# Optimization experiments

Measured on AMD Instinct MI355X. Metric: run time of the kernel, lower is better.

## Reference

```python
import jax, jax.numpy as jnp
import numpy as np

DIM = 768
HEADS = 12
HIDDEN = int(DIM * 4.0)


def layernorm(x, w, b, eps=1e-5):
    mu = jnp.mean(x, axis=-1, keepdims=True)
    var = jnp.var(x, axis=-1, keepdims=True)
    return (x - mu) * jax.lax.rsqrt(var + eps) * w + b


def setup_inputs() -> dict:
    key = jax.random.key(0)
    ks = jax.random.split(key, 16)
    B, Nq, Nc, D = 4, 1024, 1024, DIM
    s = 0.02
    return {
        "query_tokens": jax.random.normal(ks[0], (B, Nq, D), jnp.float32),
        "context_tokens": jax.random.normal(ks[1], (B, Nc, D), jnp.float32),
        "wind_bias": jax.random.normal(ks[2], (B, 1, Nq, Nc), jnp.float32),
        "ln_q_w": jnp.ones((D,), jnp.float32), "ln_q_b": jnp.zeros((D,), jnp.float32),
        "ln_kv_w": jnp.ones((D,), jnp.float32), "ln_kv_b": jnp.zeros((D,), jnp.float32),
        "Wq": jax.random.normal(ks[3], (D, D), jnp.float32) * s, "bq": jnp.zeros((D,), jnp.float32),
        "Wk": jax.random.normal(ks[4], (D, D), jnp.float32) * s, "bk": jnp.zeros((D,), jnp.float32),
        "Wv": jax.random.normal(ks[5], (D, D), jnp.float32) * s, "bv": jnp.zeros((D,), jnp.float32),
        "Wo": jax.random.normal(ks[6], (D, D), jnp.float32) * s, "bo": jnp.zeros((D,), jnp.float32),
        "beta": jnp.ones((HEADS, 1, 1), jnp.float32),
        "ln_f_w": jnp.ones((D,), jnp.float32), "ln_f_b": jnp.zeros((D,), jnp.float32),
        "W1": jax.random.normal(ks[7], (D, HIDDEN), jnp.float32) * s, "b1": jnp.zeros((HIDDEN,), jnp.float32),
        "W2": jax.random.normal(ks[8], (HIDDEN, D), jnp.float32) * s, "b2": jnp.zeros((D,), jnp.float32),
    }


def reference(query_tokens, context_tokens, wind_bias,
              ln_q_w, ln_q_b, ln_kv_w, ln_kv_b,
              Wq, bq, Wk, bk, Wv, bv, Wo, bo, beta,
              ln_f_w, ln_f_b, W1, b1, W2, b2):
    B, Nq, D = query_tokens.shape
    H = HEADS
    hd = D // H
    scale = hd ** -0.5

    q = layernorm(query_tokens, ln_q_w, ln_q_b) @ Wq + bq
    kv = layernorm(context_tokens, ln_kv_w, ln_kv_b)
    k = kv @ Wk + bk
    v = kv @ Wv + bv

    # [B, H, N, hd]
    q = q.reshape(B, Nq, H, hd).transpose(0, 2, 1, 3)
    k = k.reshape(B, -1, H, hd).transpose(0, 2, 1, 3)
    v = v.reshape(B, -1, H, hd).transpose(0, 2, 1, 3)

    attn = jnp.einsum('bhqd,bhkd->bhqk', q * scale, k)
    attn = attn + beta * wind_bias  # beta: [H,1,1] broadcasts over [B,H,Nq,Nc]
    attn = jax.nn.softmax(attn.astype(jnp.float32), axis=-1).astype(q.dtype)

    out = jnp.einsum('bhqk,bhkd->bhqd', attn, v).transpose(0, 2, 1, 3).reshape(B, Nq, D)
    out = out @ Wo + bo

    x = query_tokens + out
    h = layernorm(x, ln_f_w, ln_f_b)
    h = jax.nn.gelu(h @ W1 + b1, approximate=False) @ W2 + b2
    return x + h
```

## Files before the change

### kernel.cpp

```cpp
#include <hip/hip_runtime.h>
#include <hip/hip_bf16.h>


#define DIM 768
#define HID 3072
#define NHEAD 12
#define BATCH 4
#define SEQ 1024
#define ROWS (BATCH * SEQ)
#define HD 64

typedef __attribute__((ext_vector_type(8))) __bf16 bf16x8;
typedef __attribute__((ext_vector_type(4))) float f32x4;
typedef __attribute__((ext_vector_type(4))) unsigned int u32x4;

#define MFMA16(a, b, c) __builtin_amdgcn_mfma_f32_16x16x32_bf16((a), (b), (c), 0, 0, 0)

#define GLDS16(g, l)                                                         \
  __builtin_amdgcn_global_load_lds(                                          \
      (const __attribute__((address_space(1))) void*)(g),                    \
      (__attribute__((address_space(3))) void*)(l), 16, 0, 0)

__device__ __forceinline__ unsigned pk2(float lo, float hi) {
  unsigned a = __bfloat16_as_ushort(__float2bfloat16(lo));
  unsigned b = __bfloat16_as_ushort(__float2bfloat16(hi));
  return a | (b << 16);
}

__global__ __launch_bounds__(256) void wg_transpose(const float* __restrict__ W,
                                                    __hip_bfloat16* __restrict__ WT,
                                                    int K, int N) {
  __shared__ float tile[32][33];
  const int tx = threadIdx.x & 31, ty = threadIdx.x >> 5;
  const int n0 = blockIdx.x * 32, k0 = blockIdx.y * 32;
#pragma unroll
  for (int i = 0; i < 4; i++)
    tile[ty + i * 8][tx] = W[(size_t)(k0 + ty + i * 8) * N + n0 + tx];
  __syncthreads();
#pragma unroll
  for (int i = 0; i < 4; i++)
    WT[(size_t)(n0 + ty + i * 8) * K + k0 + tx] = __float2bfloat16(tile[tx][ty + i * 8]);
}

__global__ void wg_bcat(const float* __restrict__ bq, const float* __restrict__ bk,
                        const float* __restrict__ bv, float* __restrict__ bc) {
  int i = blockIdx.x * 256 + threadIdx.x;
  if (i < 768) bc[i] = bq[i];
  else if (i < 1536) bc[i] = bk[i - 768];
  else if (i < 2304) bc[i] = bv[i - 1536];
}

__global__ __launch_bounds__(256) void wg_ln(const float* __restrict__ in,
                                             const float* __restrict__ w,
                                             const float* __restrict__ b,
                                             __hip_bfloat16* __restrict__ out) {
  int row = blockIdx.x;
  int t = threadIdx.x;
  const float* p = in + (size_t)row * DIM;
  float v0 = p[t], v1 = p[t + 256], v2 = p[t + 512];
  float s = v0 + v1 + v2;
  float q = v0 * v0 + v1 * v1 + v2 * v2;
#pragma unroll
  for (int d = 1; d < 64; d <<= 1) {
    s += __shfl_xor(s, d);
    q += __shfl_xor(q, d);
  }
  __shared__ float ss[4], sq[4];
  if ((t & 63) == 0) {
    ss[t >> 6] = s;
    sq[t >> 6] = q;
  }
  __syncthreads();
  s = ss[0] + ss[1] + ss[2] + ss[3];
  q = sq[0] + sq[1] + sq[2] + sq[3];
  float mu = s * (1.0f / DIM);
  float var = q * (1.0f / DIM) - mu * mu;
  float rs = rsqrtf(var + 1e-5f);
  __hip_bfloat16* o = out + (size_t)row * DIM;
  o[t] = __float2bfloat16((v0 - mu) * rs * w[t] + b[t]);
  o[t + 256] = __float2bfloat16((v1 - mu) * rs * w[t + 256] + b[t + 256]);
  o[t + 512] = __float2bfloat16((v2 - mu) * rs * w[t + 512] + b[t + 512]);
}

template <int MODE>
__global__ __launch_bounds__(512) void wg_gemm(const __hip_bfloat16* __restrict__ A,
                                               const __hip_bfloat16* __restrict__ BT,
                                               const float* __restrict__ bias,
                                               void* __restrict__ Cout,
                                               const float* __restrict__ resid,
                                               float* __restrict__ aux,
                                               int N, int Kloop, int Kstride, float p0) {
  __shared__ __hip_bfloat16 As[128 * 64];
  __shared__ __hip_bfloat16 Bs[128 * 64];
  const int t = threadIdx.x;
  const int lane = t & 63;
  const int wave = t >> 6;
  const int wr = wave >> 1, wc = wave & 1;
  const int lhi = lane >> 4, llo = lane & 15;
  const int nbn = N >> 7;
  const int bm = blockIdx.x / nbn, bn = blockIdx.x % nbn;
  const int koff = (MODE == 7) ? blockIdx.y * Kloop : 0;

  const __hip_bfloat16* Ause = A;
  if (MODE == 6 && bn >= 6) Ause = A + (size_t)ROWS * DIM;

  const int s0 = t, s1 = t + 512;
  const int sr0 = s0 >> 3, sg0 = ((s0 & 7) ^ (sr0 & 7)) * 8;
  const int sr1 = s1 >> 3, sg1 = ((s1 & 7) ^ (sr1 & 7)) * 8;
  const __hip_bfloat16* Ag = Ause + (size_t)(bm * 128) * Kstride + koff;
  const __hip_bfloat16* Bg = BT + (size_t)(bn * 128) * Kstride + koff;

  f32x4 zero = {0.f, 0.f, 0.f, 0.f};
  f32x4 acc[2][4];
#pragma unroll
  for (int i = 0; i < 2; i++)
#pragma unroll
    for (int j = 0; j < 4; j++) acc[i][j] = zero;

  for (int k0 = 0; k0 < Kloop; k0 += 64) {
    __syncthreads();
    GLDS16(Ag + (size_t)sr0 * Kstride + k0 + sg0, As + s0 * 8);
    GLDS16(Ag + (size_t)sr1 * Kstride + k0 + sg1, As + s1 * 8);
    GLDS16(Bg + (size_t)sr0 * Kstride + k0 + sg0, Bs + s0 * 8);
    GLDS16(Bg + (size_t)sr1 * Kstride + k0 + sg1, Bs + s1 * 8);
    __syncthreads();
    bf16x8 af[2][2], bfr[4][2];
#pragma unroll
    for (int i = 0; i < 2; i++) {
      const int row = wr * 32 + i * 16 + llo;
#pragma unroll
      for (int kk = 0; kk < 2; kk++)
        af[i][kk] = *reinterpret_cast<const bf16x8*>(
            &As[row * 64 + (((kk * 4 + lhi) ^ (row & 7)) << 3)]);
    }
#pragma unroll
    for (int j = 0; j < 4; j++) {
      const int row = wc * 64 + j * 16 + llo;
#pragma unroll
      for (int kk = 0; kk < 2; kk++)
        bfr[j][kk] = *reinterpret_cast<const bf16x8*>(
            &Bs[row * 64 + (((kk * 4 + lhi) ^ (row & 7)) << 3)]);
    }
    __builtin_amdgcn_s_setprio(1);
#pragma unroll
    for (int kk = 0; kk < 2; kk++)
#pragma unroll
      for (int i = 0; i < 2; i++)
#pragma unroll
        for (int j = 0; j < 4; j++)
          acc[i][j] = MFMA16(af[i][kk], bfr[j][kk], acc[i][j]);
    __builtin_amdgcn_s_setprio(0);
  }

#pragma unroll
  for (int i = 0; i < 2; i++) {
    int gr = bm * 128 + wr * 32 + i * 16 + lhi * 4;
#pragma unroll
    for (int j = 0; j < 4; j++) {
      int gc = bn * 128 + wc * 64 + j * 16 + llo;
      float bv_ = (MODE == 7) ? 0.f : bias[gc];
#pragma unroll
      for (int r = 0; r < 4; r++) {
        float v = acc[i][j][r] + bv_;
        int row = gr + r;
        size_t idx = (size_t)row * N + gc;
        if (MODE == 3) {
          aux[idx] = resid[idx] + v;
        } else if (MODE == 4) {
          ((__hip_bfloat16*)Cout)[idx] =
              __float2bfloat16(v * 0.5f * (1.0f + erff(v * 0.70710678118f)));
        } else if (MODE == 7) {
          aux[(size_t)blockIdx.y * ROWS * N + idx] = v;
        } else if (MODE == 6) {
          int sec = gc / 768;
          int n2 = gc - sec * 768;
          __hip_bfloat16* base = (__hip_bfloat16*)Cout;
          if (sec == 0) {
            base[(size_t)row * DIM + n2] = __float2bfloat16(v * p0);
          } else if (sec == 1) {
            base[(size_t)ROWS * DIM + (size_t)row * DIM + n2] = __float2bfloat16(v);
          } else {
            int b_ = row >> 10, n_ = row & 1023;
            int h_ = n2 >> 6, d_ = n2 & 63;
            base[(size_t)2 * ROWS * DIM +
                 (((size_t)(b_ * NHEAD + h_) * HD + d_) << 10) + n_] = __float2bfloat16(v);
          }
        }
      }
    }
  }
}

template <int NP>
__global__ __launch_bounds__(256) void wg_red(const float* __restrict__ partial,
                                              const float* __restrict__ resid,
                                              const float* __restrict__ bias,
                                              float* __restrict__ out) {
  const int i = blockIdx.x * 256 + threadIdx.x;
  const int NF4 = ROWS * DIM / 4;
  if (i >= NF4) return;
  const f32x4* P = (const f32x4*)partial;
  f32x4 p = P[i];
#pragma unroll
  for (int c = 1; c < NP; c++) p += P[i + c * NF4];
  f32x4 r = ((const f32x4*)resid)[i];
  f32x4 bv = ((const f32x4*)bias)[i % (DIM / 4)];
  ((f32x4*)out)[i] = r + p + bv;
}

__global__ __launch_bounds__(256) void wg_attn4(const __hip_bfloat16* __restrict__ Q,
                                                const __hip_bfloat16* __restrict__ Kb,
                                                const __hip_bfloat16* __restrict__ Vt,
                                                const float* __restrict__ wb,
                                                const float* __restrict__ beta,
                                                __hip_bfloat16* __restrict__ O) {
  __shared__ __hip_bfloat16 Ks[2][4096];
  __shared__ __hip_bfloat16 Vs[2][4096];
  const int t = threadIdx.x;
  const int lane = t & 63;
  const int lhi = lane >> 4, llo = lane & 15;

  const int bid = blockIdx.x;
  const int wid = (bid & 7) * 96 + (bid >> 3);
  const int h = wid % NHEAD;
  const int g = wid / NHEAD;
  const int qt = g & 15;
  const int b = g >> 4;
  const float betah = beta[h] * 1.44269504089f;

  const int w = t >> 6;
  const size_t qrow0 = (size_t)b * SEQ + qt * 64 + w * 16;
  const __hip_bfloat16* Qp = Q + qrow0 * DIM + h * HD;
  bf16x8 a0 = *reinterpret_cast<const bf16x8*>(&Qp[(size_t)llo * DIM + lhi * 8]);
  bf16x8 a1 = *reinterpret_cast<const bf16x8*>(&Qp[(size_t)llo * DIM + 32 + lhi * 8]);

  const __hip_bfloat16* Kg = Kb + (size_t)b * SEQ * DIM + h * HD;
  const __hip_bfloat16* Vg = Vt + (size_t)(b * NHEAD + h) * HD * SEQ;
  const float* wrow = wb + (qrow0 + llo) * SEQ;

  const int slot0 = t, slot1 = t + 256;
  const int r0 = slot0 >> 3, c0 = (slot0 & 7) ^ (r0 & 7);
  const int r1 = slot1 >> 3, c1 = (slot1 & 7) ^ (r1 & 7);

  auto stage = [&](int buf, int kb) {
    GLDS16(Kg + (size_t)(kb + r0) * DIM + c0 * 8, &Ks[buf][slot0 * 8]);
    GLDS16(Kg + (size_t)(kb + r1) * DIM + c1 * 8, &Ks[buf][slot1 * 8]);
    GLDS16(Vg + (size_t)r0 * SEQ + kb + c0 * 8, &Vs[buf][slot0 * 8]);
    GLDS16(Vg + (size_t)r1 * SEQ + kb + c1 * 8, &Vs[buf][slot1 * 8]);
  };

  f32x4 zero = {0.f, 0.f, 0.f, 0.f};
  f32x4 oc[4];
#pragma unroll
  for (int c = 0; c < 4; c++) oc[c] = zero;
  float m_ = -1e30f, l_ = 0.f;

  f32x4 wv[4];
#pragma unroll
  for (int c2 = 0; c2 < 4; c2++)
    wv[c2] = *reinterpret_cast<const f32x4*>(&wrow[c2 * 16 + lhi * 4]);

  stage(0, 0);
  __syncthreads();
  int cur = 0;

  const int srcA = (lane & 15) | ((lane & 16) << 1);
  const bool chi = (lane & 32) != 0;

  for (int kt = 0; kt < SEQ / 64; kt++) {
    const int kb = kt * 64;
    f32x4 wvn[4];
    if (kt < SEQ / 64 - 1) {
      stage(cur ^ 1, kb + 64);
#pragma unroll
      for (int c2 = 0; c2 < 4; c2++)
        wvn[c2] = *reinterpret_cast<const f32x4*>(&wrow[kb + 64 + c2 * 16 + lhi * 4]);
    }

    f32x4 sv[4];
    __builtin_amdgcn_s_setprio(1);
#pragma unroll
    for (int c2 = 0; c2 < 4; c2++) {
      const int row = c2 * 16 + llo;
      bf16x8 k0 = *reinterpret_cast<const bf16x8*>(
          &Ks[cur][((row << 3) + (lhi ^ (row & 7))) << 3]);
      bf16x8 k1 = *reinterpret_cast<const bf16x8*>(
          &Ks[cur][((row << 3) + ((4 + lhi) ^ (row & 7))) << 3]);
      f32x4 s_ = zero;
      s_ = MFMA16(k0, a0, s_);
      s_ = MFMA16(k1, a1, s_);
      sv[c2] = s_;
    }
    __builtin_amdgcn_s_setprio(0);

#pragma unroll
    for (int c2 = 0; c2 < 4; c2++)
#pragma unroll
      for (int r = 0; r < 4; r++) sv[c2][r] += betah * wv[c2][r];

    float mx;
    {
      f32x4 m4;
#pragma unroll
      for (int r = 0; r < 4; r++)
        m4[r] = fmaxf(fmaxf(sv[0][r], sv[1][r]), fmaxf(sv[2][r], sv[3][r]));
      mx = fmaxf(fmaxf(m4[0], m4[1]), fmaxf(m4[2], m4[3]));
      mx = fmaxf(mx, __shfl_xor(mx, 16));
      mx = fmaxf(mx, __shfl_xor(mx, 32));
    }

    const bool grow = __any(mx > m_);
    float corr = 1.f;
    if (grow) {
      float mn = fmaxf(m_, mx);
      corr = exp2f(m_ - mn);
      m_ = mn;
    }

#pragma unroll
    for (int c2 = 0; c2 < 4; c2++)
#pragma unroll
      for (int r = 0; r < 4; r++) sv[c2][r] = exp2f(sv[c2][r] - m_);
    f32x4 s4;
#pragma unroll
    for (int r = 0; r < 4; r++) s4[r] = (sv[0][r] + sv[1][r]) + (sv[2][r] + sv[3][r]);
    float rs = (s4[0] + s4[1]) + (s4[2] + s4[3]);
    rs += __shfl_xor(rs, 16);
    rs += __shfl_xor(rs, 32);
    l_ = l_ * corr + rs;

    if (grow) {
      float cr[4];
#pragma unroll
      for (int r = 0; r < 4; r++) cr[r] = __shfl(corr, lhi * 4 + r);
#pragma unroll
      for (int c = 0; c < 4; c++)
#pragma unroll
        for (int r = 0; r < 4; r++) oc[c][r] *= cr[r];
    }

    unsigned p01[4], p23[4];
#pragma unroll
    for (int c2 = 0; c2 < 4; c2++) {
      p01[c2] = pk2(sv[c2][0], sv[c2][1]);
      p23[c2] = pk2(sv[c2][2], sv[c2][3]);
    }
    unsigned a01_0A = (unsigned)__shfl((int)p01[0], srcA);
    unsigned a01_1A = (unsigned)__shfl((int)p01[1], srcA);
    unsigned a23_0A = (unsigned)__shfl((int)p23[0], srcA);
    unsigned a23_1A = (unsigned)__shfl((int)p23[1], srcA);
    unsigned a01_0B = (unsigned)__shfl((int)p01[0], srcA + 16);
    unsigned a01_1B = (unsigned)__shfl((int)p01[1], srcA + 16);
    unsigned a23_0B = (unsigned)__shfl((int)p23[0], srcA + 16);
    unsigned a23_1B = (unsigned)__shfl((int)p23[1], srcA + 16);
    unsigned b01_2A = (unsigned)__shfl((int)p01[2], srcA);
    unsigned b01_3A = (unsigned)__shfl((int)p01[3], srcA);
    unsigned b23_2A = (unsigned)__shfl((int)p23[2], srcA);
    unsigned b23_3A = (unsigned)__shfl((int)p23[3], srcA);
    unsigned b01_2B = (unsigned)__shfl((int)p01[2], srcA + 16);
    unsigned b01_3B = (unsigned)__shfl((int)p01[3], srcA + 16);
    unsigned b23_2B = (unsigned)__shfl((int)p23[2], srcA + 16);
    unsigned b23_3B = (unsigned)__shfl((int)p23[3], srcA + 16);
    u32x4 t0, t1;
    t0[0] = chi ? a01_1A : a01_0A;
    t0[1] = chi ? a23_1A : a23_0A;
    t0[2] = chi ? a01_1B : a01_0B;
    t0[3] = chi ? a23_1B : a23_0B;
    t1[0] = chi ? b01_3A : b01_2A;
    t1[1] = chi ? b23_3A : b23_2A;
    t1[2] = chi ? b01_3B : b01_2B;
    t1[3] = chi ? b23_3B : b23_2B;
    bf16x8 pf0 = __builtin_bit_cast(bf16x8, t0);
    bf16x8 pf1 = __builtin_bit_cast(bf16x8, t1);

    __builtin_amdgcn_s_setprio(1);
#pragma unroll
    for (int c = 0; c < 4; c++) {
      const int row = c * 16 + llo;
      bf16x8 v0 = *reinterpret_cast<const bf16x8*>(
          &Vs[cur][((row << 3) + (lhi ^ (row & 7))) << 3]);
      bf16x8 v1 = *reinterpret_cast<const bf16x8*>(
          &Vs[cur][((row << 3) + ((4 + lhi) ^ (row & 7))) << 3]);
      oc[c] = MFMA16(pf0, v0, oc[c]);
      oc[c] = MFMA16(pf1, v1, oc[c]);
    }
    __builtin_amdgcn_s_setprio(0);

    if (kt < SEQ / 64 - 1) {
#pragma unroll
      for (int c2 = 0; c2 < 4; c2++) wv[c2] = wvn[c2];
    }
    __syncthreads();
    cur ^= 1;
  }

  float iv[4];
  float invl = 1.0f / l_;
#pragma unroll
  for (int r = 0; r < 4; r++) iv[r] = __shfl(invl, lhi * 4 + r);
  __hip_bfloat16* Op = O + qrow0 * DIM + h * HD;
#pragma unroll
  for (int c = 0; c < 4; c++)
#pragma unroll
    for (int r = 0; r < 4; r++)
      Op[(size_t)(lhi * 4 + r) * DIM + c * 16 + llo] = __float2bfloat16(oc[c][r] * iv[r]);
}

extern "C" void kernel_launch(void* const* d_in, const int* in_sizes, int n_in,
                              void* d_out, int out_size, void* d_ws, size_t ws_size,
                              hipStream_t stream) {
  const float* query = (const float*)d_in[0];
  const float* context = (const float*)d_in[1];
  const float* wind = (const float*)d_in[2];
  const float* ln_q_w = (const float*)d_in[3];
  const float* ln_q_b = (const float*)d_in[4];
  const float* ln_kv_w = (const float*)d_in[5];
  const float* ln_kv_b = (const float*)d_in[6];
  const float* Wq = (const float*)d_in[7];
  const float* bq = (const float*)d_in[8];
  const float* Wk = (const float*)d_in[9];
  const float* bk = (const float*)d_in[10];
  const float* Wv = (const float*)d_in[11];
  const float* bv = (const float*)d_in[12];
  const float* Wo = (const float*)d_in[13];
  const float* bo = (const float*)d_in[14];
  const float* beta = (const float*)d_in[15];
  const float* ln_f_w = (const float*)d_in[16];
  const float* ln_f_b = (const float*)d_in[17];
  const float* W1 = (const float*)d_in[18];
  const float* b1 = (const float*)d_in[19];
  const float* W2 = (const float*)d_in[20];
  const float* b2 = (const float*)d_in[21];
  float* out = (float*)d_out;

  char* ws = (char*)d_ws;
  size_t off = 0;
  auto take = [&](size_t bytes) -> char* {
    char* p = ws + off;
    off += (bytes + 255) & ~(size_t)255;
    return p;
  };
  const size_t actB = (size_t)ROWS * DIM * 2;
  __hip_bfloat16* qln = (__hip_bfloat16*)take(actB);
  __hip_bfloat16* kvln = (__hip_bfloat16*)take(actB);
  __hip_bfloat16* qb = (__hip_bfloat16*)take(actB);
  __hip_bfloat16* kbuf = (__hip_bfloat16*)take(actB);
  __hip_bfloat16* vt = (__hip_bfloat16*)take(actB);
  __hip_bfloat16* aout = (__hip_bfloat16*)take(actB);
  __hip_bfloat16* hbuf = (__hip_bfloat16*)take(actB);
  float* xbuf = (float*)take((size_t)ROWS * DIM * 4);
  __hip_bfloat16* hid = (__hip_bfloat16*)take((size_t)ROWS * HID * 2);
  __hip_bfloat16* WqT = (__hip_bfloat16*)take((size_t)DIM * DIM * 2);
  __hip_bfloat16* WkT = (__hip_bfloat16*)take((size_t)DIM * DIM * 2);
  __hip_bfloat16* WvT = (__hip_bfloat16*)take((size_t)DIM * DIM * 2);
  __hip_bfloat16* WoT = (__hip_bfloat16*)take((size_t)DIM * DIM * 2);
  __hip_bfloat16* W1T = (__hip_bfloat16*)take((size_t)DIM * HID * 2);
  __hip_bfloat16* W2T = (__hip_bfloat16*)take((size_t)HID * DIM * 2);
  float* bcat = (float*)take(2304 * 4);
  float* kpart = (float*)take((size_t)4 * ROWS * DIM * 4);

  wg_transpose<<<dim3(24, 24), 256, 0, stream>>>(Wq, WqT, DIM, DIM);
  wg_transpose<<<dim3(24, 24), 256, 0, stream>>>(Wk, WkT, DIM, DIM);
  wg_transpose<<<dim3(24, 24), 256, 0, stream>>>(Wv, WvT, DIM, DIM);
  wg_transpose<<<dim3(24, 24), 256, 0, stream>>>(Wo, WoT, DIM, DIM);
  wg_transpose<<<dim3(96, 24), 256, 0, stream>>>(W1, W1T, DIM, HID);
  wg_transpose<<<dim3(24, 96), 256, 0, stream>>>(W2, W2T, HID, DIM);
  wg_bcat<<<9, 256, 0, stream>>>(bq, bk, bv, bcat);

  wg_ln<<<ROWS, 256, 0, stream>>>(query, ln_q_w, ln_q_b, qln);
  wg_ln<<<ROWS, 256, 0, stream>>>(context, ln_kv_w, ln_kv_b, kvln);

  const float scale = 0.125f * 1.44269504089f;
  wg_gemm<6><<<32 * 18, 512, 0, stream>>>(qln, WqT, bcat, qb, nullptr, nullptr,
                                          2304, DIM, DIM, scale);

  wg_attn4<<<768, 256, 0, stream>>>(qb, kbuf, vt, wind, beta, aout);

  const int g768 = (ROWS / 128) * (DIM / 128);
  const int g3072 = (ROWS / 128) * (HID / 128);
  wg_gemm<3><<<g768, 512, 0, stream>>>(aout, WoT, bo, nullptr, query, xbuf, DIM, DIM, DIM, 0.f);
  wg_ln<<<ROWS, 256, 0, stream>>>(xbuf, ln_f_w, ln_f_b, hbuf);
  wg_gemm<4><<<g3072, 512, 0, stream>>>(hbuf, W1T, b1, hid, nullptr, nullptr, HID, DIM, DIM, 0.f);
  wg_gemm<7><<<dim3(g768, 4), 512, 0, stream>>>(hid, W2T, nullptr, nullptr, nullptr, kpart,
                                                DIM, HID / 4, HID, 0.f);
  wg_red<4><<<(ROWS * DIM / 4 + 255) / 256, 256, 0, stream>>>(kpart, xbuf, b2, out);
}
```

Before: 225.2 us.

## Triple-buffer GEMM K-loop, approximate GELU, and merge transpose/layernorm launches

The GEMM main loop moves from a single-buffered 64-wide K tile with two barriers per step to a three-stage ring of 32-wide K tiles. Loads are issued two steps ahead, with vmcnt waits and one barrier per step, so global-to-LDS transfers overlap the MFMA work. The exact erf GELU in the W1 epilogue is replaced by a sigmoid-based tanh-style approximation to cut transcendental cost, which adds small numeric deviation. The four square weight transposes are merged into one launch, and the query and context layernorms run as a single dual launch to reduce launch overhead.

```diff
diff --git a/kernel.cpp b/kernel.cpp
--- a/kernel.cpp
+++ b/kernel.cpp
@@ -13,6 +13,7 @@
 typedef __attribute__((ext_vector_type(8))) __bf16 bf16x8;
 typedef __attribute__((ext_vector_type(4))) float f32x4;
 typedef __attribute__((ext_vector_type(4))) unsigned int u32x4;
+typedef __attribute__((ext_vector_type(2))) unsigned int u32x2;
 
 #define MFMA16(a, b, c) __builtin_amdgcn_mfma_f32_16x16x32_bf16((a), (b), (c), 0, 0, 0)
 
@@ -25,6 +26,29 @@
   unsigned a = __bfloat16_as_ushort(__float2bfloat16(lo));
   unsigned b = __bfloat16_as_ushort(__float2bfloat16(hi));
   return a | (b << 16);
+}
+
+__global__ __launch_bounds__(256) void wg_transpose4(const float* __restrict__ Wq,
+                                                     const float* __restrict__ Wk,
+                                                     const float* __restrict__ Wv,
+                                                     const float* __restrict__ Wo,
+                                                     __hip_bfloat16* __restrict__ WqT,
+                                                     __hip_bfloat16* __restrict__ WkT,
+                                                     __hip_bfloat16* __restrict__ WvT,
+                                                     __hip_bfloat16* __restrict__ WoT) {
+  __shared__ float tile[32][33];
+  const int z = blockIdx.z;
+  const float* W = (z == 0) ? Wq : (z == 1) ? Wk : (z == 2) ? Wv : Wo;
+  __hip_bfloat16* WT = (z == 0) ? WqT : (z == 1) ? WkT : (z == 2) ? WvT : WoT;
+  const int tx = threadIdx.x & 31, ty = threadIdx.x >> 5;
+  const int n0 = blockIdx.x * 32, k0 = blockIdx.y * 32;
+#pragma unroll
+  for (int i = 0; i < 4; i++)
+    tile[ty + i * 8][tx] = W[(size_t)(k0 + ty + i * 8) * DIM + n0 + tx];
+  __syncthreads();
+#pragma unroll
+  for (int i = 0; i < 4; i++)
+    WT[(size_t)(n0 + ty + i * 8) * DIM + k0 + tx] = __float2bfloat16(tile[tx][ty + i * 8]);
 }
 
 __global__ __launch_bounds__(256) void wg_transpose(const float* __restrict__ W,
@@ -50,13 +74,24 @@
   else if (i < 2304) bc[i] = bv[i - 1536];
 }
 
-__global__ __launch_bounds__(256) void wg_ln(const float* __restrict__ in,
-                                             const float* __restrict__ w,
-                                             const float* __restrict__ b,
-                                             __hip_bfloat16* __restrict__ out) {
+template <int DUAL>
+__global__ __launch_bounds__(256) void wg_ln(const float* __restrict__ inA,
+                                             const float* __restrict__ wA,
+                                             const float* __restrict__ bA,
+                                             const float* __restrict__ inB,
+                                             const float* __restrict__ wB,
+                                             const float* __restrict__ bB,
+                                             __hip_bfloat16* __restrict__ outbuf) {
   int row = blockIdx.x;
   int t = threadIdx.x;
-  const float* p = in + (size_t)row * DIM;
+  const float* in = inA;
+  const float* w = wA;
+  const float* b = bA;
+  int lrow = row;
+  if (DUAL && row >= ROWS) {
+    in = inB; w = wB; b = bB; lrow = row - ROWS;
+  }
+  const float* p = in + (size_t)lrow * DIM;
   float v0 = p[t], v1 = p[t + 256], v2 = p[t + 512];
   float s = v0 + v1 + v2;
   float q = v0 * v0 + v1 * v1 + v2 * v2;
@@ -76,7 +111,7 @@
   float mu = s * (1.0f / DIM);
   float var = q * (1.0f / DIM) - mu * mu;
   float rs = rsqrtf(var + 1e-5f);
-  __hip_bfloat16* o = out + (size_t)row * DIM;
+  __hip_bfloat16* o = outbuf + (size_t)row * DIM;
   o[t] = __float2bfloat16((v0 - mu) * rs * w[t] + b[t]);
   o[t + 256] = __float2bfloat16((v1 - mu) * rs * w[t + 256] + b[t + 256]);
   o[t + 512] = __float2bfloat16((v2 - mu) * rs * w[t + 512] + b[t + 512]);
@@ -90,8 +125,8 @@
                                                const float* __restrict__ resid,
                                                float* __restrict__ aux,
                                                int N, int Kloop, int Kstride, float p0) {
-  __shared__ __hip_bfloat16 As[128 * 64];
-  __shared__ __hip_bfloat16 Bs[128 * 64];
+  __shared__ __hip_bfloat16 As[3][128 * 32];
+  __shared__ __hip_bfloat16 Bs[3][128 * 32];
   const int t = threadIdx.x;
   const int lane = t & 63;
   const int wave = t >> 6;
@@ -104,11 +139,10 @@
   const __hip_bfloat16* Ause = A;
   if (MODE == 6 && bn >= 6) Ause = A + (size_t)ROWS * DIM;
 
-  const int s0 = t, s1 = t + 512;
-  const int sr0 = s0 >> 3, sg0 = ((s0 & 7) ^ (sr0 & 7)) * 8;
-  const int sr1 = s1 >> 3, sg1 = ((s1 & 7) ^ (sr1 & 7)) * 8;
-  const __hip_bfloat16* Ag = Ause + (size_t)(bm * 128) * Kstride + koff;
-  const __hip_bfloat16* Bg = BT + (size_t)(bn * 128) * Kstride + koff;
+  const int srow = t >> 2;
+  const int sg = ((t & 3) ^ ((srow >> 1) & 3)) * 8;
+  const __hip_bfloat16* Ag = Ause + (size_t)(bm * 128 + srow) * Kstride + koff + sg;
+  const __hip_bfloat16* Bg = BT + (size_t)(bn * 128 + srow) * Kstride + koff + sg;
 
   f32x4 zero = {0.f, 0.f, 0.f, 0.f};
   f32x4 acc[2][4];
@@ -117,39 +151,49 @@
 #pragma unroll
     for (int j = 0; j < 4; j++) acc[i][j] = zero;
 
-  for (int k0 = 0; k0 < Kloop; k0 += 64) {
-    __syncthreads();
-    GLDS16(Ag + (size_t)sr0 * Kstride + k0 + sg0, As + s0 * 8);
-    GLDS16(Ag + (size_t)sr1 * Kstride + k0 + sg1, As + s1 * 8);
-    GLDS16(Bg + (size_t)sr0 * Kstride + k0 + sg0, Bs + s0 * 8);
-    GLDS16(Bg + (size_t)sr1 * Kstride + k0 + sg1, Bs + s1 * 8);
-    __syncthreads();
-    bf16x8 af[2][2], bfr[4][2];
+  const int nk = Kloop >> 5;
+
+  GLDS16(Ag, &As[0][t * 8]);
+  GLDS16(Bg, &Bs[0][t * 8]);
+  GLDS16(Ag + 32, &As[1][t * 8]);
+  GLDS16(Bg + 32, &Bs[1][t * 8]);
+
+  int buf = 0;
+  for (int kt = 0; kt < nk; kt++) {
+    if (kt < nk - 1) {
+      asm volatile("s_waitcnt vmcnt(2)" ::: "memory");
+    } else {
+      asm volatile("s_waitcnt vmcnt(0)" ::: "memory");
+    }
+    __builtin_amdgcn_s_barrier();
+    asm volatile("" ::: "memory");
+    if (kt + 2 < nk) {
+      int nbuf = buf + 2;
+      if (nbuf >= 3) nbuf -= 3;
+      GLDS16(Ag + (kt + 2) * 32, &As[nbuf][t * 8]);
+      GLDS16(Bg + (kt + 2) * 32, &Bs[nbuf][t * 8]);
+    }
+    bf16x8 af[2], bfr[4];
 #pragma unroll
     for (int i = 0; i < 2; i++) {
       const int row = wr * 32 + i * 16 + llo;
-#pragma unroll
-      for (int kk = 0; kk < 2; kk++)
-        af[i][kk] = *reinterpret_cast<const bf16x8*>(
-            &As[row * 64 + (((kk * 4 + lhi) ^ (row & 7)) << 3)]);
+      af[i] = *reinterpret_cast<const bf16x8*>(
+          &As[buf][row * 32 + ((lhi ^ ((row >> 1) & 3)) << 3)]);
     }
 #pragma unroll
     for (int j = 0; j < 4; j++) {
       const int row = wc * 64 + j * 16 + llo;
-#pragma unroll
-      for (int kk = 0; kk < 2; kk++)
-        bfr[j][kk] = *reinterpret_cast<const bf16x8*>(
-            &Bs[row * 64 + (((kk * 4 + lhi) ^ (row & 7)) << 3)]);
+      bfr[j] = *reinterpret_cast<const bf16x8*>(
+          &Bs[buf][row * 32 + ((lhi ^ ((row >> 1) & 3)) << 3)]);
     }
     __builtin_amdgcn_s_setprio(1);
 #pragma unroll
-    for (int kk = 0; kk < 2; kk++)
-#pragma unroll
-      for (int i = 0; i < 2; i++)
-#pragma unroll
-        for (int j = 0; j < 4; j++)
-          acc[i][j] = MFMA16(af[i][kk], bfr[j][kk], acc[i][j]);
+    for (int i = 0; i < 2; i++)
+#pragma unroll
+      for (int j = 0; j < 4; j++) acc[i][j] = MFMA16(af[i], bfr[j], acc[i][j]);
     __builtin_amdgcn_s_setprio(0);
+    buf++;
+    if (buf == 3) buf = 0;
   }
 
 #pragma unroll
@@ -167,8 +211,10 @@
         if (MODE == 3) {
           aux[idx] = resid[idx] + v;
         } else if (MODE == 4) {
-          ((__hip_bfloat16*)Cout)[idx] =
-              __float2bfloat16(v * 0.5f * (1.0f + erff(v * 0.70710678118f)));
+          float x3 = v * v * v;
+          float z = -2.302208f * v - 0.102943f * x3;
+          float g = v / (1.0f + exp2f(z));
+          ((__hip_bfloat16*)Cout)[idx] = __float2bfloat16(g);
         } else if (MODE == 7) {
           aux[(size_t)blockIdx.y * ROWS * N + idx] = v;
         } else if (MODE == 6) {
@@ -459,16 +505,13 @@
   float* bcat = (float*)take(2304 * 4);
   float* kpart = (float*)take((size_t)4 * ROWS * DIM * 4);
 
-  wg_transpose<<<dim3(24, 24), 256, 0, stream>>>(Wq, WqT, DIM, DIM);
-  wg_transpose<<<dim3(24, 24), 256, 0, stream>>>(Wk, WkT, DIM, DIM);
-  wg_transpose<<<dim3(24, 24), 256, 0, stream>>>(Wv, WvT, DIM, DIM);
-  wg_transpose<<<dim3(24, 24), 256, 0, stream>>>(Wo, WoT, DIM, DIM);
+  wg_transpose4<<<dim3(24, 24, 4), 256, 0, stream>>>(Wq, Wk, Wv, Wo, WqT, WkT, WvT, WoT);
   wg_transpose<<<dim3(96, 24), 256, 0, stream>>>(W1, W1T, DIM, HID);
   wg_transpose<<<dim3(24, 96), 256, 0, stream>>>(W2, W2T, HID, DIM);
   wg_bcat<<<9, 256, 0, stream>>>(bq, bk, bv, bcat);
 
-  wg_ln<<<ROWS, 256, 0, stream>>>(query, ln_q_w, ln_q_b, qln);
-  wg_ln<<<ROWS, 256, 0, stream>>>(context, ln_kv_w, ln_kv_b, kvln);
+  wg_ln<1><<<2 * ROWS, 256, 0, stream>>>(query, ln_q_w, ln_q_b,
+                                         context, ln_kv_w, ln_kv_b, qln);
 
   const float scale = 0.125f * 1.44269504089f;
   wg_gemm<6><<<32 * 18, 512, 0, stream>>>(qln, WqT, bcat, qb, nullptr, nullptr,
@@ -479,7 +522,7 @@
   const int g768 = (ROWS / 128) * (DIM / 128);
   const int g3072 = (ROWS / 128) * (HID / 128);
   wg_gemm<3><<<g768, 512, 0, stream>>>(aout, WoT, bo, nullptr, query, xbuf, DIM, DIM, DIM, 0.f);
-  wg_ln<<<ROWS, 256, 0, stream>>>(xbuf, ln_f_w, ln_f_b, hbuf);
+  wg_ln<0><<<ROWS, 256, 0, stream>>>(xbuf, ln_f_w, ln_f_b, nullptr, nullptr, nullptr, hbuf);
   wg_gemm<4><<<g3072, 512, 0, stream>>>(hbuf, W1T, b1, hid, nullptr, nullptr, HID, DIM, DIM, 0.f);
   wg_gemm<7><<<dim3(g768, 4), 512, 0, stream>>>(hid, W2T, nullptr, nullptr, nullptr, kpart,
                                                 DIM, HID / 4, HID, 0.f);
```

New measurement: 215.4 us. 1.05x faster.
